# Performance work log

Measured on AMD Instinct MI355X. Metric: run time of the kernel, lower is better.

The kernel has to match this reference:

```python
import jax, jax.numpy as jnp
import numpy as np

N_NODES = 20000
N_EDGES = 200000
F = 132            # features_dim
DEGREES = (1, 2, 3)
REPEATS = jnp.array([3, 5, 7])   # 2l+1
EV_DIM = 15
H_INV, D_INV = 4, 33   # num_heads, inv_head_dim
H_EV, D_EV = 3, 44     # len(degrees), ev_head_dim
NRB = 32


def so3_invariants(x, y):
    # per-degree inner product over the (2l+1) components -> [E, len(degrees)]
    p = x * y
    return jnp.stack([p[:, 0:3].sum(-1), p[:, 3:8].sum(-1), p[:, 8:15].sum(-1)], axis=-1)


def filter_net(rbf, evi, Wr1, br1, Wr2, br2, We1, be1, We2, be2):
    # mlp_rbf: Linear(nrb,F)->SiLU->Linear(F,F); mlp_ev: Linear(3,F//4)->SiLU->Linear(F//4,F)
    r = jax.nn.silu(rbf @ Wr1 + br1) @ Wr2 + br2
    e = jax.nn.silu(evi @ We1 + be1) @ We2 + be2
    return r + e


def setup_inputs() -> dict:
    key = jax.random.key(0)
    ks = jax.random.split(key, 32)
    s = 0.05
    inp = {
        'inv_features': jax.random.normal(ks[0], (N_NODES, F), jnp.float32),
        'ev_features': jax.random.normal(ks[1], (N_NODES, EV_DIM), jnp.float32),
        'rbf': jax.random.uniform(ks[2], (N_EDGES, NRB), jnp.float32),
        'senders': jax.random.randint(ks[3], (N_EDGES,), 0, N_NODES, jnp.int32),
        'receivers': jax.random.randint(ks[4], (N_EDGES,), 0, N_NODES, jnp.int32),
        'sh_vectors': jax.random.normal(ks[5], (N_EDGES, EV_DIM), jnp.float32),
        'cutoffs': jax.random.uniform(ks[6], (N_EDGES, 1), jnp.float32),
        # attention weights
        'W_q_inv': jax.random.normal(ks[7], (H_INV, D_INV, D_INV), jnp.float32) * s,
        'W_k_inv': jax.random.normal(ks[8], (H_INV, D_INV, D_INV), jnp.float32) * s,
        'W_v_inv': jax.random.normal(ks[9], (H_INV, D_INV, D_INV), jnp.float32) * s,
        'W_q_ev': jax.random.normal(ks[10], (H_EV, D_EV, D_EV), jnp.float32) * s,
        'W_k_ev': jax.random.normal(ks[11], (H_EV, D_EV, D_EV), jnp.float32) * s,
    }
    # two FilterNets (inv and ev), stored as [in,out] matrices
    for tag, base in (('fi', 12), ('fe', 20)):
        inp[f'{tag}_rbf_W1'] = jax.random.normal(ks[base + 0], (NRB, F), jnp.float32) * s
        inp[f'{tag}_rbf_b1'] = jnp.zeros((F,), jnp.float32)
        inp[f'{tag}_rbf_W2'] = jax.random.normal(ks[base + 1], (F, F), jnp.float32) * s
        inp[f'{tag}_rbf_b2'] = jnp.zeros((F,), jnp.float32)
        inp[f'{tag}_ev_W1'] = jax.random.normal(ks[base + 2], (len(DEGREES), F // 4), jnp.float32) * s
        inp[f'{tag}_ev_b1'] = jnp.zeros((F // 4,), jnp.float32)
        inp[f'{tag}_ev_W2'] = jax.random.normal(ks[base + 3], (F // 4, F), jnp.float32) * s
        inp[f'{tag}_ev_b2'] = jnp.zeros((F,), jnp.float32)
    # interaction block linear: (F+len(degrees)) -> (F+len(degrees))
    inp['W_int'] = jax.random.normal(ks[28], (F + len(DEGREES), F + len(DEGREES)), jnp.float32) * s
    inp['b_int'] = jnp.zeros((F + len(DEGREES),), jnp.float32)
    return inp


def _forward(inv_features, ev_features, rbf, sh_vectors, cutoffs,
             W_q_inv, W_k_inv, W_v_inv, W_q_ev, W_k_ev,
             fi, fe, W_int, b_int, senders, receivers):
    E = rbf.shape[0]
    N = inv_features.shape[0]
    # ---- EuclideanAttentionBlock ----
    ev_diff = ev_features[senders] - ev_features[receivers]          # [E, 15]
    evi = so3_invariants(ev_diff, ev_diff)                            # [E, 3]
    fw_inv = filter_net(rbf, evi, *fi).reshape(E, H_INV, D_INV)
    fw_ev = filter_net(rbf, evi, *fe).reshape(E, H_EV, D_EV)
    x_inv = inv_features.reshape(N, H_INV, D_INV)
    x_ev = inv_features.reshape(N, H_EV, D_EV)
    q_inv = jnp.einsum('Hij,NHi->NHj', W_q_inv, x_inv)[receivers]
    k_inv = jnp.einsum('Hij,NHi->NHj', W_k_inv, x_inv)[senders]
    v_inv = jnp.einsum('Hij,NHi->NHj', W_v_inv, x_inv)[senders]
    q_ev = jnp.einsum('Hij,NHi->NHj', W_q_ev, x_ev)[receivers]
    k_ev = jnp.einsum('Hij,NHi->NHj', W_k_ev, x_ev)[senders]
    alpha_inv = (q_inv * k_inv * fw_inv).sum(-1, keepdims=True) / np.sqrt(D_INV)  # [E,H,1]
    scaled_inv = cutoffs[:, None] * alpha_inv * v_inv                 # [E,H,D]
    d_inv = jax.ops.segment_sum(scaled_inv, receivers, num_segments=N).reshape(N, F)
    alpha_ev = (q_ev * k_ev * fw_ev).sum(-1) / np.sqrt(D_EV)          # [E,3]
    alpha_ev = jnp.repeat(alpha_ev, REPEATS, axis=-1, total_repeat_length=EV_DIM)
    d_ev = jax.ops.segment_sum(cutoffs * alpha_ev * sh_vectors, receivers, num_segments=N)
    att_inv = inv_features + d_inv
    att_ev = ev_features + d_ev
    # ---- InteractionBlock ----
    evi2 = so3_invariants(att_ev, att_ev)                             # [N,3]
    t = jnp.concatenate([att_inv, evi2], axis=-1) @ W_int + b_int
    d_inv2, b_ev = t[:, :F], t[:, F:]
    d_ev2 = jnp.repeat(b_ev, REPEATS, axis=-1, total_repeat_length=EV_DIM) * att_ev
    return att_inv + d_inv2, att_ev + d_ev2


def reference(inv_features, ev_features, rbf, senders, receivers, sh_vectors, cutoffs,
              W_q_inv, W_k_inv, W_v_inv, W_q_ev, W_k_ev,
              fi_rbf_W1, fi_rbf_b1, fi_rbf_W2, fi_rbf_b2, fi_ev_W1, fi_ev_b1, fi_ev_W2, fi_ev_b2,
              fe_rbf_W1, fe_rbf_b1, fe_rbf_W2, fe_rbf_b2, fe_ev_W1, fe_ev_b1, fe_ev_W2, fe_ev_b2,
              W_int, b_int):
    fi = (fi_rbf_W1, fi_rbf_b1, fi_rbf_W2, fi_rbf_b2, fi_ev_W1, fi_ev_b1, fi_ev_W2, fi_ev_b2)
    fe = (fe_rbf_W1, fe_rbf_b1, fe_rbf_W2, fe_rbf_b2, fe_ev_W1, fe_ev_b1, fe_ev_W2, fe_ev_b2)
    return _forward(inv_features, ev_features, rbf, sh_vectors, cutoffs,
                    W_q_inv, W_k_inv, W_v_inv, W_q_ev, W_k_ev,
                    fi, fe, W_int, b_int, senders, receivers)
```

## Files before the change

kernel.cpp:

```cpp
#include <hip/hip_runtime.h>


#define NN 20000
#define NE 200000
#define FD 132
#define RB 32
#define EVD 15
#define TE 64
#define KPAD 200
#define KG 192
#define NP 144
#define PNT 28
#define FNT 28

typedef __attribute__((ext_vector_type(8))) short bf16x8;
typedef __attribute__((ext_vector_type(4))) float f32x4;

__device__ __forceinline__ float silu_f(float x) {
    return x / (1.0f + __expf(-x));
}
__device__ __forceinline__ unsigned short f2bf(float x) {
    union { float f; unsigned u; } v; v.f = x;
    unsigned r = v.u + 0x7FFF + ((v.u >> 16) & 1);
    return (unsigned short)(r >> 16);
}

__global__ __launch_bounds__(256) void k_prep(
    const float* __restrict__ Wq, const float* __restrict__ Wk, const float* __restrict__ Wv,
    const float* __restrict__ fiW1, const float* __restrict__ fiW2, const float* __restrict__ fiWe2,
    const float* __restrict__ feW1, const float* __restrict__ feW2, const float* __restrict__ feWe2,
    unsigned short* __restrict__ W1Tfi, unsigned short* __restrict__ W1Tfe,
    unsigned short* __restrict__ W2Tfi, unsigned short* __restrict__ W2Tfe,
    float* __restrict__ WqP, float* __restrict__ WkP, float* __restrict__ WvP)
{
    const int gid = blockIdx.x * 256 + threadIdx.x;
    const int gs  = gridDim.x * 256;
    for (int idx = gid; idx < NP * RB; idx += gs) {
        int n = idx / RB, k = idx - n * RB;
        W1Tfi[idx] = f2bf((n < FD) ? fiW1[k * FD + n] : 0.0f);
        W1Tfe[idx] = f2bf((n < FD) ? feW1[k * FD + n] : 0.0f);
    }
    for (int idx = gid; idx < NP * KG; idx += gs) {
        int n = idx / KG, k = idx - n * KG;
        float vi = 0.0f, ve = 0.0f;
        if (n < FD) {
            if (k < FD)       { vi = fiW2[k * FD + n];          ve = feW2[k * FD + n]; }
            else if (k < 165) { vi = fiWe2[(k - FD) * FD + n];  ve = feWe2[(k - FD) * FD + n]; }
        }
        W2Tfi[idx] = f2bf(vi);
        W2Tfe[idx] = f2bf(ve);
    }
    for (int idx = gid; idx < 4 * 33 * 36; idx += gs) {
        int H = idx / (33 * 36), rem = idx - H * (33 * 36);
        int i = rem / 36, jp = rem - i * 36;
        float q = 0.f, k = 0.f, v = 0.f;
        if (jp < 33) {
            q = Wq[H * 1089 + i * 33 + jp];
            k = Wk[H * 1089 + i * 33 + jp];
            v = Wv[H * 1089 + i * 33 + jp];
        }
        WqP[idx] = q; WkP[idx] = k; WvP[idx] = v;
    }
}

__global__ __launch_bounds__(256) void k_hist(const int* __restrict__ rcv,
                                              int* __restrict__ cnt)
{
    int e = blockIdx.x * 256 + threadIdx.x;
    if (e < NE) atomicAdd(&cnt[rcv[e]], 1);
}

__global__ __launch_bounds__(256) void k_scan(int* __restrict__ cnt_cursor,
                                              int* __restrict__ roff)
{
    __shared__ int buf[256];
    __shared__ int carry_s;
    const int t = threadIdx.x;
    if (t == 0) carry_s = 0;
    __syncthreads();
    for (int base = 0; base < NN; base += 256) {
        int v = (base + t < NN) ? cnt_cursor[base + t] : 0;
        buf[t] = v;
        __syncthreads();
        for (int off = 1; off < 256; off <<= 1) {
            int add = (t >= off) ? buf[t - off] : 0;
            __syncthreads();
            buf[t] += add;
            __syncthreads();
        }
        int ex = carry_s + buf[t] - v;
        if (base + t < NN) { roff[base + t] = ex; cnt_cursor[base + t] = ex; }
        __syncthreads();
        if (t == 0) carry_s += buf[255];
        __syncthreads();
    }
    if (t == 0) roff[NN] = carry_s;
}

__global__ __launch_bounds__(256) void k_fill(const int* __restrict__ rcv,
                                              int* __restrict__ cursor,
                                              int* __restrict__ eid)
{
    int e = blockIdx.x * 256 + threadIdx.x;
    if (e < NE) {
        int p = atomicAdd(&cursor[rcv[e]], 1);
        eid[p] = e;
    }
}

__device__ __forceinline__ void proj_inv_pass(
    const float* __restrict__ wb, const float (*__restrict__ xT)[PNT],
    float* __restrict__ outp, int t, int n0)
{
    const int q = t % 36, g = t / 36;
    if (g >= 7) return;
    const int H = q / 9, jb = (q - H * 9) * 4, nb = g * 4;
    const int fb = H * 33;
    float acc[4][4] = {};
    for (int i = 0; i < 33; ++i) {
        const float4 w = *(const float4*)&wb[(fb + i) * 36 + jb];
        const float4 x = *(const float4*)&xT[fb + i][nb];
        const float xs[4] = {x.x, x.y, x.z, x.w};
        const float ws[4] = {w.x, w.y, w.z, w.w};
        #pragma unroll
        for (int r = 0; r < 4; ++r)
            #pragma unroll
            for (int c = 0; c < 4; ++c)
                acc[r][c] = fmaf(ws[c], xs[r], acc[r][c]);
    }
    #pragma unroll
    for (int c = 0; c < 4; ++c) {
        int jj = jb + c;
        if (jj >= 33) break;
        int j = H * 33 + jj;
        #pragma unroll
        for (int r = 0; r < 4; ++r) {
            int n = n0 + nb + r;
            if (n < NN) outp[n * FD + j] = acc[r][c];
        }
    }
}

__device__ __forceinline__ void proj_ev_pass(
    const float* __restrict__ wb, const float (*__restrict__ xT)[PNT],
    float* __restrict__ outp, int t, int n0)
{
    const int q = t % 33, g = t / 33;
    if (g >= 7) return;
    const int H = q / 11, jb = (q - H * 11) * 4, nb = g * 4;
    const int fb = H * 44;
    float acc[4][4] = {};
    for (int i = 0; i < 44; ++i) {
        const float4 w = *(const float4*)&wb[(fb + i) * 44 + jb];
        const float4 x = *(const float4*)&xT[fb + i][nb];
        const float xs[4] = {x.x, x.y, x.z, x.w};
        const float ws[4] = {w.x, w.y, w.z, w.w};
        #pragma unroll
        for (int r = 0; r < 4; ++r)
            #pragma unroll
            for (int c = 0; c < 4; ++c)
                acc[r][c] = fmaf(ws[c], xs[r], acc[r][c]);
    }
    #pragma unroll
    for (int c = 0; c < 4; ++c) {
        int j = fb + jb + c;
        #pragma unroll
        for (int r = 0; r < 4; ++r) {
            int n = n0 + nb + r;
            if (n < NN) outp[n * FD + j] = acc[r][c];
        }
    }
}

__global__ __launch_bounds__(256) void k_proj(
    const float* __restrict__ xin,
    const float* __restrict__ WqP, const float* __restrict__ WkP, const float* __restrict__ WvP,
    const float* __restrict__ Wqe, const float* __restrict__ Wke,
    float* __restrict__ qinv, float* __restrict__ kinv, float* __restrict__ vinv,
    float* __restrict__ qev, float* __restrict__ kev)
{
    __shared__ __align__(16) float xT[FD][PNT];
    __shared__ __align__(16) float wb[5808];
    const int t = threadIdx.x;
    const int n0 = blockIdx.x * PNT;

    for (int idx = t; idx < PNT * FD; idx += 256) {
        int nl = idx / FD, j = idx - nl * FD;
        int n = n0 + nl;
        xT[j][nl] = (n < NN) ? xin[n * FD + j] : 0.0f;
    }
    for (int idx = t; idx < 4752; idx += 256) wb[idx] = WqP[idx];
    __syncthreads();
    proj_inv_pass(wb, xT, qinv, t, n0);
    __syncthreads();
    for (int idx = t; idx < 4752; idx += 256) wb[idx] = WkP[idx];
    __syncthreads();
    proj_inv_pass(wb, xT, kinv, t, n0);
    __syncthreads();
    for (int idx = t; idx < 4752; idx += 256) wb[idx] = WvP[idx];
    __syncthreads();
    proj_inv_pass(wb, xT, vinv, t, n0);
    __syncthreads();
    for (int idx = t; idx < 5808; idx += 256) wb[idx] = Wqe[idx];
    __syncthreads();
    proj_ev_pass(wb, xT, qev, t, n0);
    __syncthreads();
    for (int idx = t; idx < 5808; idx += 256) wb[idx] = Wke[idx];
    __syncthreads();
    proj_ev_pass(wb, xT, kev, t, n0);
}

__global__ __launch_bounds__(256) void k_evi(
    const float* __restrict__ ev, const int* __restrict__ snd,
    const int* __restrict__ rcv, float* __restrict__ evi)
{
    int e = blockIdx.x * 256 + threadIdx.x;
    if (e >= NE) return;
    int s = snd[e], r = rcv[e];
    const float* ps = &ev[s * EVD];
    const float* pr = &ev[r * EVD];
    float s0 = 0.f, s1 = 0.f, s2 = 0.f;
    #pragma unroll
    for (int m = 0; m < 3; ++m)  { float d = ps[m] - pr[m]; s0 = fmaf(d, d, s0); }
    #pragma unroll
    for (int m = 3; m < 8; ++m)  { float d = ps[m] - pr[m]; s1 = fmaf(d, d, s1); }
    #pragma unroll
    for (int m = 8; m < 15; ++m) { float d = ps[m] - pr[m]; s2 = fmaf(d, d, s2); }
    evi[e * 3 + 0] = s0; evi[e * 3 + 1] = s1; evi[e * 3 + 2] = s2;
}

template<int PATH>
__global__ __launch_bounds__(256, 4) void k_edge(
    const float* __restrict__ rbf, const float* __restrict__ evi,
    const int* __restrict__ snd, const int* __restrict__ rcv,
    const float* __restrict__ cut,
    const unsigned short* __restrict__ W1T,
    const float* __restrict__ b1,
    const unsigned short* __restrict__ W2T,
    const float* __restrict__ b2,
    const float* __restrict__ We1, const float* __restrict__ be1,
    const float* __restrict__ be2,
    const float* __restrict__ qt, const float* __restrict__ kt,
    float* __restrict__ aout)
{
    __shared__ __align__(16) char lds_buf[TE * FD * 4];
    __shared__ float evl[TE * 3];
    __shared__ int   sl[TE];
    __shared__ int   rl[TE];
    __shared__ float cl[TE];

    typedef unsigned short (*HTp)[KPAD];
    HTp HT   = (HTp)lds_buf;
    float* FW = (float*)lds_buf;

    const int t    = threadIdx.x;
    const int wv   = t >> 6;
    const int ln   = t & 63;
    const int lrow = ln & 15;
    const int kseg = ln >> 4;
    const int e0   = blockIdx.x * TE;

    if (t < TE) {
        sl[t] = snd[e0 + t];
        rl[t] = rcv[e0 + t];
        cl[t] = cut[e0 + t];
    }
    for (int idx = t; idx < TE * 3; idx += 256) evl[idx] = evi[e0 * 3 + idx];
    __syncthreads();

    {
        const int erow = e0 + 16 * wv + lrow;
        const float4 ra = *(const float4*)&rbf[erow * RB + kseg * 8];
        const float4 rb = *(const float4*)&rbf[erow * RB + kseg * 8 + 4];
        bf16x8 afrag;
        afrag[0] = (short)f2bf(ra.x); afrag[1] = (short)f2bf(ra.y);
        afrag[2] = (short)f2bf(ra.z); afrag[3] = (short)f2bf(ra.w);
        afrag[4] = (short)f2bf(rb.x); afrag[5] = (short)f2bf(rb.y);
        afrag[6] = (short)f2bf(rb.z); afrag[7] = (short)f2bf(rb.w);
        #pragma unroll
        for (int nt = 0; nt < 9; ++nt) {
            const int ncol = nt * 16 + lrow;
            bf16x8 bfrag = *(const bf16x8*)&W1T[ncol * RB + kseg * 8];
            f32x4 acc = {0.f, 0.f, 0.f, 0.f};
            acc = __builtin_amdgcn_mfma_f32_16x16x32_bf16(afrag, bfrag, acc, 0, 0, 0);
            if (ncol < FD) {
                const float bias = b1[ncol];
                #pragma unroll
                for (int r = 0; r < 4; ++r)
                    HT[16 * wv + kseg * 4 + r][ncol] = f2bf(silu_f(acc[r] + bias));
            }
        }
    }
    for (int idx = t; idx < TE * 33; idx += 256) {
        int e = idx / 33, ii = idx - e * 33;
        float a = be1[ii];
        a = fmaf(evl[e * 3 + 0], We1[ii], a);
        a = fmaf(evl[e * 3 + 1], We1[33 + ii], a);
        a = fmaf(evl[e * 3 + 2], We1[66 + ii], a);
        HT[e][FD + ii] = f2bf(silu_f(a));
    }
    for (int idx = t; idx < TE * (KPAD - 165); idx += 256) {
        int e = idx / (KPAD - 165), kk = idx - e * (KPAD - 165);
        HT[e][165 + kk] = 0;
    }
    __syncthreads();

    f32x4 acc[9];
    #pragma unroll
    for (int nt = 0; nt < 9; ++nt) acc[nt] = (f32x4){0.f, 0.f, 0.f, 0.f};
    {
        const unsigned short* hrow = &HT[16 * wv + lrow][0];
        #pragma unroll
        for (int kt = 0; kt < 6; ++kt) {
            bf16x8 afrag = *(const bf16x8*)&hrow[kt * 32 + kseg * 8];
            #pragma unroll
            for (int nt = 0; nt < 9; ++nt) {
                bf16x8 bfrag = *(const bf16x8*)&W2T[(nt * 16 + lrow) * KG + kt * 32 + kseg * 8];
                acc[nt] = __builtin_amdgcn_mfma_f32_16x16x32_bf16(afrag, bfrag, acc[nt], 0, 0, 0);
            }
        }
    }
    __syncthreads();

    #pragma unroll
    for (int nt = 0; nt < 9; ++nt) {
        const int ncol = nt * 16 + lrow;
        if (ncol < FD) {
            const float bias = b2[ncol] + be2[ncol];
            #pragma unroll
            for (int r = 0; r < 4; ++r)
                FW[(16 * wv + kseg * 4 + r) * FD + ncol] = acc[nt][r] + bias;
        }
    }
    __syncthreads();

    for (int idx = t; idx < TE * FD; idx += 256) {
        int e = idx / FD, j = idx - e * FD;
        FW[idx] *= qt[rl[e] * FD + j] * kt[sl[e] * FD + j];
    }
    __syncthreads();

    if (PATH == 0) {
        int e = t >> 2, H = t & 3;
        const float* fp = &FW[e * FD + H * 33];
        float a = 0.0f;
        #pragma unroll
        for (int j = 0; j < 33; ++j) a += fp[j];
        aout[(e0 + e) * 4 + H] = a * cl[e] * 0.17407765595569785f;
    } else {
        if (t < TE * 3) {
            int e = t / 3, H = t - e * 3;
            const float* fp = &FW[e * FD + H * 44];
            float a = 0.0f;
            #pragma unroll
            for (int j = 0; j < 44; ++j) a += fp[j];
            aout[(e0 + e) * 4 + H] = a * cl[e] * 0.15075567228888181f;
        }
    }
}

__global__ __launch_bounds__(256) void k_final(
    const float* __restrict__ xin, const float* __restrict__ evf,
    const float* __restrict__ vt, const float* __restrict__ sh,
    const float* __restrict__ alphaI, const float* __restrict__ alphaE,
    const int* __restrict__ roff, const int* __restrict__ eid,
    const int* __restrict__ snd,
    const float* __restrict__ Wint, const float* __restrict__ bint,
    float* __restrict__ out)
{
    __shared__ __align__(16) float catT[136][FNT];
    __shared__ __align__(16) float wb[45 * 136];
    __shared__ float aev[FNT][16];
    __shared__ float tacc[FNT][4];
    const int t = threadIdx.x;
    const int n0 = blockIdx.x * FNT;
    const int wv = t >> 6, ln = t & 63;

    const int h0 = ln / 33;
    const int h1 = (64 + ln) / 33;
    const int hm = (ln < 3) ? 0 : ((ln < 8) ? 1 : 2);
    for (int nl = wv; nl < FNT; nl += 4) {
        const int n = n0 + nl;
        float a0 = 0.f, a1 = 0.f, a2 = 0.f, dv = 0.f;
        if (n < NN) {
            const int pend = roff[n + 1];
            for (int p = roff[n]; p < pend; ++p) {
                const int e = eid[p];
                const int s = snd[e];
                const float* vrow = vt + s * FD;
                a0 = fmaf(alphaI[e * 4 + h0], vrow[ln], a0);
                a1 = fmaf(alphaI[e * 4 + h1], vrow[64 + ln], a1);
                if (ln < 4)  a2 = fmaf(alphaI[e * 4 + 3], vrow[128 + ln], a2);
                if (ln < 15) dv = fmaf(alphaE[e * 4 + hm], sh[e * EVD + ln], dv);
            }
            catT[ln][nl]      = xin[n * FD + ln]      + a0;
            catT[64 + ln][nl] = xin[n * FD + 64 + ln] + a1;
            if (ln < 4)  catT[128 + ln][nl] = xin[n * FD + 128 + ln] + a2;
            if (ln < 15) aev[nl][ln] = evf[n * EVD + ln] + dv;
        } else {
            catT[ln][nl] = 0.f; catT[64 + ln][nl] = 0.f;
            if (ln < 4)  catT[128 + ln][nl] = 0.f;
            if (ln < 15) aev[nl][ln] = 0.f;
        }
    }
    if (t < FNT) catT[135][t] = 0.0f;
    __syncthreads();
    if (t < FNT * 3) {
        int nl = t / 3, k = t - nl * 3;
        int lo = (k == 0) ? 0 : ((k == 1) ? 3 : 8);
        int hi = (k == 0) ? 3 : ((k == 1) ? 8 : 15);
        float s = 0.f;
        for (int m = lo; m < hi; ++m) { float v = aev[nl][m]; s = fmaf(v, v, s); }
        catT[FD + k][nl] = s;
    }

    const int q = t % 34, g = t / 34;
    const int jb = q * 4, nb = g * 4;
    const bool act = (g < 7);
    float acc[4][4] = {};
    for (int ch = 0; ch < 3; ++ch) {
        __syncthreads();
        const int rbase = ch * 45;
        for (int idx = t; idx < 45 * 136; idx += 256) {
            int r = idx / 136, j = idx - r * 136;
            wb[idx] = (j < 135) ? Wint[(rbase + r) * 135 + j] : 0.0f;
        }
        __syncthreads();
        if (act) {
            for (int c = 0; c < 45; ++c) {
                const float4 w = *(const float4*)&wb[c * 136 + jb];
                const float4 x = *(const float4*)&catT[rbase + c][nb];
                const float xs[4] = {x.x, x.y, x.z, x.w};
                const float ws[4] = {w.x, w.y, w.z, w.w};
                #pragma unroll
                for (int r = 0; r < 4; ++r)
                    #pragma unroll
                    for (int cc = 0; cc < 4; ++cc)
                        acc[r][cc] = fmaf(ws[cc], xs[r], acc[r][cc]);
            }
        }
    }
    if (act) {
        #pragma unroll
        for (int c = 0; c < 4; ++c) {
            int j = jb + c;
            if (j >= 135) break;
            float bj = bint[j];
            #pragma unroll
            for (int r = 0; r < 4; ++r) {
                int n = n0 + nb + r;
                if (n >= NN) continue;
                float a = acc[r][c] + bj;
                if (j < FD) out[n * FD + j] = catT[j][nb + r] + a;
                else        tacc[nb + r][j - FD] = a;
            }
        }
    }
    __syncthreads();
    for (int idx = t; idx < FNT * EVD; idx += 256) {
        int nl = idx / EVD, m = idx - nl * EVD;
        int n = n0 + nl;
        if (n >= NN) continue;
        int hd = (m < 3) ? 0 : ((m < 8) ? 1 : 2);
        out[NN * FD + n * EVD + m] = aev[nl][m] * (1.0f + tacc[nl][hd]);
    }
}

extern "C" void kernel_launch(void* const* d_in, const int* in_sizes, int n_in,
                              void* d_out, int out_size, void* d_ws, size_t ws_size,
                              hipStream_t stream)
{
    (void)in_sizes; (void)n_in; (void)out_size; (void)ws_size;
    const float* xin  = (const float*)d_in[0];
    const float* evf  = (const float*)d_in[1];
    const float* rbf  = (const float*)d_in[2];
    const int*   snd  = (const int*)d_in[3];
    const int*   rcv  = (const int*)d_in[4];
    const float* sh   = (const float*)d_in[5];
    const float* cut  = (const float*)d_in[6];
    const float* Wint = (const float*)d_in[28];
    const float* bint = (const float*)d_in[29];

    float* ws     = (float*)d_ws;
    float* qinv   = ws;
    float* kinv   = qinv   + NN * FD;
    float* vinv   = kinv   + NN * FD;
    float* qev    = vinv   + NN * FD;
    float* kev    = qev    + NN * FD;
    float* evi    = kev    + NN * FD;
    float* alphaI = evi    + NE * 3;
    float* alphaE = alphaI + NE * 4;
    int*   iwork  = (int*)(alphaE + NE * 4);
    int*   roff   = iwork;
    int*   cnt_cursor = roff + (NN + 1);
    int*   eid    = cnt_cursor + NN;
    float* wtail  = (float*)(iwork + 240004);

    unsigned short* W2Tfi = (unsigned short*)wtail;
    unsigned short* W2Tfe = W2Tfi + NP * KG;
    unsigned short* W1Tfi = W2Tfe + NP * KG;
    unsigned short* W1Tfe = W1Tfi + NP * RB;
    float* WqP = (float*)(W1Tfe + NP * RB);
    float* WkP = WqP + 4 * 33 * 36;
    float* WvP = WkP + 4 * 33 * 36;

    hipMemsetAsync(cnt_cursor, 0, (size_t)NN * sizeof(int), stream);
    k_hist<<<(NE + 255) / 256, 256, 0, stream>>>(rcv, cnt_cursor);
    k_scan<<<1, 256, 0, stream>>>(cnt_cursor, roff);
    k_fill<<<(NE + 255) / 256, 256, 0, stream>>>(rcv, cnt_cursor, eid);

    k_prep<<<64, 256, 0, stream>>>(
        (const float*)d_in[7], (const float*)d_in[8], (const float*)d_in[9],
        (const float*)d_in[12], (const float*)d_in[14], (const float*)d_in[18],
        (const float*)d_in[20], (const float*)d_in[22], (const float*)d_in[26],
        W1Tfi, W1Tfe, W2Tfi, W2Tfe, WqP, WkP, WvP);

    k_proj<<<(NN + PNT - 1) / PNT, 256, 0, stream>>>(
        xin, WqP, WkP, WvP,
        (const float*)d_in[10], (const float*)d_in[11],
        qinv, kinv, vinv, qev, kev);
    k_evi<<<(NE + 255) / 256, 256, 0, stream>>>(evf, snd, rcv, evi);

    const int nt = NE / TE;
    k_edge<0><<<nt, 256, 0, stream>>>(rbf, evi, snd, rcv, cut,
        W1Tfi, (const float*)d_in[13], W2Tfi, (const float*)d_in[15],
        (const float*)d_in[16], (const float*)d_in[17], (const float*)d_in[19],
        qinv, kinv, alphaI);
    k_edge<1><<<nt, 256, 0, stream>>>(rbf, evi, snd, rcv, cut,
        W1Tfe, (const float*)d_in[21], W2Tfe, (const float*)d_in[23],
        (const float*)d_in[24], (const float*)d_in[25], (const float*)d_in[27],
        qev, kev, alphaE);

    k_final<<<(NN + FNT - 1) / FNT, 256, 0, stream>>>(
        xin, evf, vinv, sh, alphaI, alphaE, roff, eid, snd,
        Wint, bint, (float*)d_out);
}
```

Measured before the change: 763.9 us.

## Process edges in receiver-sorted order and restructure scan, edge reduction, final GEMM

```diff
diff --git a/kernel.cpp b/kernel.cpp
--- a/kernel.cpp
+++ b/kernel.cpp
@@ -70,31 +70,35 @@
     if (e < NE) atomicAdd(&cnt[rcv[e]], 1);
 }
 
-__global__ __launch_bounds__(256) void k_scan(int* __restrict__ cnt_cursor,
-                                              int* __restrict__ roff)
-{
-    __shared__ int buf[256];
-    __shared__ int carry_s;
+__global__ __launch_bounds__(1024) void k_scan(int* __restrict__ cnt_cursor,
+                                               int* __restrict__ roff)
+{
+    __shared__ int sums[1024];
     const int t = threadIdx.x;
-    if (t == 0) carry_s = 0;
-    __syncthreads();
-    for (int base = 0; base < NN; base += 256) {
-        int v = (base + t < NN) ? cnt_cursor[base + t] : 0;
-        buf[t] = v;
+    const int base = t * 20;
+    int loc[20];
+    int s = 0;
+    #pragma unroll
+    for (int i = 0; i < 20; ++i) {
+        int idx = base + i;
+        int v = (idx < NN) ? cnt_cursor[idx] : 0;
+        loc[i] = s; s += v;
+    }
+    sums[t] = s;
+    __syncthreads();
+    for (int off = 1; off < 1024; off <<= 1) {
+        int v2 = (t >= off) ? sums[t - off] : 0;
         __syncthreads();
-        for (int off = 1; off < 256; off <<= 1) {
-            int add = (t >= off) ? buf[t - off] : 0;
-            __syncthreads();
-            buf[t] += add;
-            __syncthreads();
-        }
-        int ex = carry_s + buf[t] - v;
-        if (base + t < NN) { roff[base + t] = ex; cnt_cursor[base + t] = ex; }
+        sums[t] += v2;
         __syncthreads();
-        if (t == 0) carry_s += buf[255];
-        __syncthreads();
-    }
-    if (t == 0) roff[NN] = carry_s;
+    }
+    int ex = (t > 0) ? sums[t - 1] : 0;
+    #pragma unroll
+    for (int i = 0; i < 20; ++i) {
+        int idx = base + i;
+        if (idx < NN) { roff[idx] = ex + loc[i]; cnt_cursor[idx] = ex + loc[i]; }
+    }
+    if (t == 1023) roff[NN] = sums[1023];
 }
 
 __global__ __launch_bounds__(256) void k_fill(const int* __restrict__ rcv,
@@ -106,6 +110,30 @@
         int p = atomicAdd(&cursor[rcv[e]], 1);
         eid[p] = e;
     }
+}
+
+__global__ __launch_bounds__(256) void k_eprep(
+    const float* __restrict__ ev, const int* __restrict__ snd,
+    const int* __restrict__ rcv, const float* __restrict__ cut,
+    const int* __restrict__ eid,
+    float* __restrict__ evi_s, float* __restrict__ cut_s,
+    int* __restrict__ ss, int* __restrict__ rs)
+{
+    int p = blockIdx.x * 256 + threadIdx.x;
+    if (p >= NE) return;
+    int e = eid[p];
+    int s = snd[e], r = rcv[e];
+    ss[p] = s; rs[p] = r; cut_s[p] = cut[e];
+    const float* ps = &ev[s * EVD];
+    const float* pr = &ev[r * EVD];
+    float s0 = 0.f, s1 = 0.f, s2 = 0.f;
+    #pragma unroll
+    for (int m = 0; m < 3; ++m)  { float d = ps[m] - pr[m]; s0 = fmaf(d, d, s0); }
+    #pragma unroll
+    for (int m = 3; m < 8; ++m)  { float d = ps[m] - pr[m]; s1 = fmaf(d, d, s1); }
+    #pragma unroll
+    for (int m = 8; m < 15; ++m) { float d = ps[m] - pr[m]; s2 = fmaf(d, d, s2); }
+    evi_s[p * 3 + 0] = s0; evi_s[p * 3 + 1] = s1; evi_s[p * 3 + 2] = s2;
 }
 
 __device__ __forceinline__ void proj_inv_pass(
@@ -210,30 +238,11 @@
     proj_ev_pass(wb, xT, kev, t, n0);
 }
 
-__global__ __launch_bounds__(256) void k_evi(
-    const float* __restrict__ ev, const int* __restrict__ snd,
-    const int* __restrict__ rcv, float* __restrict__ evi)
-{
-    int e = blockIdx.x * 256 + threadIdx.x;
-    if (e >= NE) return;
-    int s = snd[e], r = rcv[e];
-    const float* ps = &ev[s * EVD];
-    const float* pr = &ev[r * EVD];
-    float s0 = 0.f, s1 = 0.f, s2 = 0.f;
-    #pragma unroll
-    for (int m = 0; m < 3; ++m)  { float d = ps[m] - pr[m]; s0 = fmaf(d, d, s0); }
-    #pragma unroll
-    for (int m = 3; m < 8; ++m)  { float d = ps[m] - pr[m]; s1 = fmaf(d, d, s1); }
-    #pragma unroll
-    for (int m = 8; m < 15; ++m) { float d = ps[m] - pr[m]; s2 = fmaf(d, d, s2); }
-    evi[e * 3 + 0] = s0; evi[e * 3 + 1] = s1; evi[e * 3 + 2] = s2;
-}
-
 template<int PATH>
 __global__ __launch_bounds__(256, 4) void k_edge(
-    const float* __restrict__ rbf, const float* __restrict__ evi,
-    const int* __restrict__ snd, const int* __restrict__ rcv,
-    const float* __restrict__ cut,
+    const float* __restrict__ rbf, const float* __restrict__ evi_s,
+    const int* __restrict__ eid, const int* __restrict__ ss,
+    const int* __restrict__ rs, const float* __restrict__ cut_s,
     const unsigned short* __restrict__ W1T,
     const float* __restrict__ b1,
     const unsigned short* __restrict__ W2T,
@@ -243,6 +252,9 @@
     const float* __restrict__ qt, const float* __restrict__ kt,
     float* __restrict__ aout)
 {
+    constexpr int   DH = (PATH == 0) ? 33 : 44;
+    constexpr float SC = (PATH == 0) ? 0.17407765595569785f : 0.15075567228888181f;
+
     __shared__ __align__(16) char lds_buf[TE * FD * 4];
     __shared__ float evl[TE * 3];
     __shared__ int   sl[TE];
@@ -250,7 +262,7 @@
     __shared__ float cl[TE];
 
     typedef unsigned short (*HTp)[KPAD];
-    HTp HT   = (HTp)lds_buf;
+    HTp HT    = (HTp)lds_buf;
     float* FW = (float*)lds_buf;
 
     const int t    = threadIdx.x;
@@ -258,20 +270,22 @@
     const int ln   = t & 63;
     const int lrow = ln & 15;
     const int kseg = ln >> 4;
-    const int e0   = blockIdx.x * TE;
+    const int p0   = blockIdx.x * TE;
+
+    const int  prow = p0 + 16 * wv + lrow;
+    const int  eorg = eid[prow];
+    const float4 ra = *(const float4*)&rbf[(size_t)eorg * RB + kseg * 8];
+    const float4 rb = *(const float4*)&rbf[(size_t)eorg * RB + kseg * 8 + 4];
 
     if (t < TE) {
-        sl[t] = snd[e0 + t];
-        rl[t] = rcv[e0 + t];
-        cl[t] = cut[e0 + t];
-    }
-    for (int idx = t; idx < TE * 3; idx += 256) evl[idx] = evi[e0 * 3 + idx];
+        sl[t] = ss[p0 + t];
+        rl[t] = rs[p0 + t];
+        cl[t] = cut_s[p0 + t];
+    }
+    for (int idx = t; idx < TE * 3; idx += 256) evl[idx] = evi_s[p0 * 3 + idx];
     __syncthreads();
 
     {
-        const int erow = e0 + 16 * wv + lrow;
-        const float4 ra = *(const float4*)&rbf[erow * RB + kseg * 8];
-        const float4 rb = *(const float4*)&rbf[erow * RB + kseg * 8 + 4];
         bf16x8 afrag;
         afrag[0] = (short)f2bf(ra.x); afrag[1] = (short)f2bf(ra.y);
         afrag[2] = (short)f2bf(ra.z); afrag[3] = (short)f2bf(ra.w);
@@ -334,27 +348,29 @@
     }
     __syncthreads();
 
-    for (int idx = t; idx < TE * FD; idx += 256) {
-        int e = idx / FD, j = idx - e * FD;
-        FW[idx] *= qt[rl[e] * FD + j] * kt[sl[e] * FD + j];
-    }
-    __syncthreads();
-
-    if (PATH == 0) {
-        int e = t >> 2, H = t & 3;
-        const float* fp = &FW[e * FD + H * 33];
-        float a = 0.0f;
-        #pragma unroll
-        for (int j = 0; j < 33; ++j) a += fp[j];
-        aout[(e0 + e) * 4 + H] = a * cl[e] * 0.17407765595569785f;
-    } else {
-        if (t < TE * 3) {
-            int e = t / 3, H = t - e * 3;
-            const float* fp = &FW[e * FD + H * 44];
-            float a = 0.0f;
-            #pragma unroll
-            for (int j = 0; j < 44; ++j) a += fp[j];
-            aout[(e0 + e) * 4 + H] = a * cl[e] * 0.15075567228888181f;
+    {
+        const int eq = t >> 2;
+        const int m  = t & 3;
+        const int jb = m * 33;
+        const float* qp = qt + (size_t)rl[eq] * FD + jb;
+        const float* kp = kt + (size_t)sl[eq] * FD + jb;
+        const float* fp = &FW[eq * FD + jb];
+        const int hlo   = jb / DH;
+        const int split = (PATH == 0) ? 33 : (DH * (hlo + 1) - jb);
+        float pa = 0.f, pb = 0.f;
+        #pragma unroll
+        for (int jj = 0; jj < 33; ++jj) {
+            float f = fp[jj] * qp[jj] * kp[jj];
+            if (jj < split) pa += f; else pb += f;
+        }
+        float nxt = __shfl_down(pa, 1);
+        if (PATH == 0) {
+            aout[(size_t)(p0 + eq) * 4 + m] = pa * cl[eq] * SC;
+        } else {
+            if (m < 3) {
+                float a = ((m == 0) ? pa : pb) + nxt;
+                aout[(size_t)(p0 + eq) * 4 + m] = a * cl[eq] * SC;
+            }
         }
     }
 }
@@ -364,12 +380,11 @@
     const float* __restrict__ vt, const float* __restrict__ sh,
     const float* __restrict__ alphaI, const float* __restrict__ alphaE,
     const int* __restrict__ roff, const int* __restrict__ eid,
-    const int* __restrict__ snd,
+    const int* __restrict__ ss,
     const float* __restrict__ Wint, const float* __restrict__ bint,
     float* __restrict__ out)
 {
     __shared__ __align__(16) float catT[136][FNT];
-    __shared__ __align__(16) float wb[45 * 136];
     __shared__ float aev[FNT][16];
     __shared__ float tacc[FNT][4];
     const int t = threadIdx.x;
@@ -384,14 +399,35 @@
         float a0 = 0.f, a1 = 0.f, a2 = 0.f, dv = 0.f;
         if (n < NN) {
             const int pend = roff[n + 1];
-            for (int p = roff[n]; p < pend; ++p) {
-                const int e = eid[p];
-                const int s = snd[e];
-                const float* vrow = vt + s * FD;
-                a0 = fmaf(alphaI[e * 4 + h0], vrow[ln], a0);
-                a1 = fmaf(alphaI[e * 4 + h1], vrow[64 + ln], a1);
-                if (ln < 4)  a2 = fmaf(alphaI[e * 4 + 3], vrow[128 + ln], a2);
-                if (ln < 15) dv = fmaf(alphaE[e * 4 + hm], sh[e * EVD + ln], dv);
+            int p = roff[n];
+            for (; p + 2 <= pend; p += 2) {
+                const int sA = ss[p], sB = ss[p + 1];
+                const int eA = eid[p], eB = eid[p + 1];
+                const float* vA = vt + (size_t)sA * FD;
+                const float* vB = vt + (size_t)sB * FD;
+                const float aA0 = alphaI[(size_t)p * 4 + h0];
+                const float aB0 = alphaI[(size_t)(p + 1) * 4 + h0];
+                const float aA1 = alphaI[(size_t)p * 4 + h1];
+                const float aB1 = alphaI[(size_t)(p + 1) * 4 + h1];
+                a0 = fmaf(aA0, vA[ln], a0);      a0 = fmaf(aB0, vB[ln], a0);
+                a1 = fmaf(aA1, vA[64 + ln], a1); a1 = fmaf(aB1, vB[64 + ln], a1);
+                if (ln < 4) {
+                    a2 = fmaf(alphaI[(size_t)p * 4 + 3], vA[128 + ln], a2);
+                    a2 = fmaf(alphaI[(size_t)(p + 1) * 4 + 3], vB[128 + ln], a2);
+                }
+                if (ln < 15) {
+                    dv = fmaf(alphaE[(size_t)p * 4 + hm], sh[(size_t)eA * EVD + ln], dv);
+                    dv = fmaf(alphaE[(size_t)(p + 1) * 4 + hm], sh[(size_t)eB * EVD + ln], dv);
+                }
+            }
+            for (; p < pend; ++p) {
+                const int sA = ss[p];
+                const int eA = eid[p];
+                const float* vA = vt + (size_t)sA * FD;
+                a0 = fmaf(alphaI[(size_t)p * 4 + h0], vA[ln], a0);
+                a1 = fmaf(alphaI[(size_t)p * 4 + h1], vA[64 + ln], a1);
+                if (ln < 4)  a2 = fmaf(alphaI[(size_t)p * 4 + 3], vA[128 + ln], a2);
+                if (ln < 15) dv = fmaf(alphaE[(size_t)p * 4 + hm], sh[(size_t)eA * EVD + ln], dv);
             }
             catT[ln][nl]      = xin[n * FD + ln]      + a0;
             catT[64 + ln][nl] = xin[n * FD + 64 + ln] + a1;
@@ -413,34 +449,30 @@
         for (int m = lo; m < hi; ++m) { float v = aev[nl][m]; s = fmaf(v, v, s); }
         catT[FD + k][nl] = s;
     }
+    __syncthreads();
 
     const int q = t % 34, g = t / 34;
     const int jb = q * 4, nb = g * 4;
     const bool act = (g < 7);
     float acc[4][4] = {};
-    for (int ch = 0; ch < 3; ++ch) {
-        __syncthreads();
-        const int rbase = ch * 45;
-        for (int idx = t; idx < 45 * 136; idx += 256) {
-            int r = idx / 136, j = idx - r * 136;
-            wb[idx] = (j < 135) ? Wint[(rbase + r) * 135 + j] : 0.0f;
-        }
-        __syncthreads();
-        if (act) {
-            for (int c = 0; c < 45; ++c) {
-                const float4 w = *(const float4*)&wb[c * 136 + jb];
-                const float4 x = *(const float4*)&catT[rbase + c][nb];
-                const float xs[4] = {x.x, x.y, x.z, x.w};
-                const float ws[4] = {w.x, w.y, w.z, w.w};
-                #pragma unroll
-                for (int r = 0; r < 4; ++r)
-                    #pragma unroll
-                    for (int cc = 0; cc < 4; ++cc)
-                        acc[r][cc] = fmaf(ws[cc], xs[r], acc[r][cc]);
-            }
-        }
-    }
     if (act) {
+        #pragma unroll 5
+        for (int c = 0; c < 135; ++c) {
+            const float* wr = Wint + c * 135 + jb;
+            const float w0 = wr[0];
+            const float w1 = wr[1];
+            const float w2 = wr[2];
+            const float w3 = (jb + 3 < 135) ? wr[3] : 0.f;
+            const float4 x = *(const float4*)&catT[c][nb];
+            const float xs[4] = {x.x, x.y, x.z, x.w};
+            #pragma unroll
+            for (int r = 0; r < 4; ++r) {
+                acc[r][0] = fmaf(w0, xs[r], acc[r][0]);
+                acc[r][1] = fmaf(w1, xs[r], acc[r][1]);
+                acc[r][2] = fmaf(w2, xs[r], acc[r][2]);
+                acc[r][3] = fmaf(w3, xs[r], acc[r][3]);
+            }
+        }
         #pragma unroll
         for (int c = 0; c < 4; ++c) {
             int j = jb + c;
@@ -487,14 +519,17 @@
     float* vinv   = kinv   + NN * FD;
     float* qev    = vinv   + NN * FD;
     float* kev    = qev    + NN * FD;
-    float* evi    = kev    + NN * FD;
-    float* alphaI = evi    + NE * 3;
+    float* alphaI = kev    + NN * FD;
     float* alphaE = alphaI + NE * 4;
-    int*   iwork  = (int*)(alphaE + NE * 4);
+    float* evi_s  = alphaE + NE * 4;
+    float* cut_s  = evi_s  + NE * 3;
+    int*   iwork  = (int*)(cut_s + NE);
     int*   roff   = iwork;
     int*   cnt_cursor = roff + (NN + 1);
     int*   eid    = cnt_cursor + NN;
-    float* wtail  = (float*)(iwork + 240004);
+    int*   ss     = eid + NE;
+    int*   rs     = ss + NE;
+    float* wtail  = (float*)(iwork + 640004);
 
     unsigned short* W2Tfi = (unsigned short*)wtail;
     unsigned short* W2Tfe = W2Tfi + NP * KG;
@@ -506,8 +541,10 @@
 
     hipMemsetAsync(cnt_cursor, 0, (size_t)NN * sizeof(int), stream);
     k_hist<<<(NE + 255) / 256, 256, 0, stream>>>(rcv, cnt_cursor);
-    k_scan<<<1, 256, 0, stream>>>(cnt_cursor, roff);
+    k_scan<<<1, 1024, 0, stream>>>(cnt_cursor, roff);
     k_fill<<<(NE + 255) / 256, 256, 0, stream>>>(rcv, cnt_cursor, eid);
+    k_eprep<<<(NE + 255) / 256, 256, 0, stream>>>(evf, snd, rcv, cut, eid,
+                                                  evi_s, cut_s, ss, rs);
 
     k_prep<<<64, 256, 0, stream>>>(
         (const float*)d_in[7], (const float*)d_in[8], (const float*)d_in[9],
@@ -519,19 +556,18 @@
         xin, WqP, WkP, WvP,
         (const float*)d_in[10], (const float*)d_in[11],
         qinv, kinv, vinv, qev, kev);
-    k_evi<<<(NE + 255) / 256, 256, 0, stream>>>(evf, snd, rcv, evi);
 
     const int nt = NE / TE;
-    k_edge<0><<<nt, 256, 0, stream>>>(rbf, evi, snd, rcv, cut,
+    k_edge<0><<<nt, 256, 0, stream>>>(rbf, evi_s, eid, ss, rs, cut_s,
         W1Tfi, (const float*)d_in[13], W2Tfi, (const float*)d_in[15],
         (const float*)d_in[16], (const float*)d_in[17], (const float*)d_in[19],
         qinv, kinv, alphaI);
-    k_edge<1><<<nt, 256, 0, stream>>>(rbf, evi, snd, rcv, cut,
+    k_edge<1><<<nt, 256, 0, stream>>>(rbf, evi_s, eid, ss, rs, cut_s,
         W1Tfe, (const float*)d_in[21], W2Tfe, (const float*)d_in[23],
         (const float*)d_in[24], (const float*)d_in[25], (const float*)d_in[27],
         qev, kev, alphaE);
 
     k_final<<<(NN + FNT - 1) / FNT, 256, 0, stream>>>(
-        xin, evf, vinv, sh, alphaI, alphaE, roff, eid, snd,
+        xin, evf, vinv, sh, alphaI, alphaE, roff, eid, ss,
         Wint, bint, (float*)d_out);
 }
```

Measured after the change: 657.8 us. -13.9%, faster.
